# Kernel tuning notes

Measured on AMD Instinct MI355X. Metric: run time of the kernel, lower is better.

## Reference

```python
import jax, jax.numpy as jnp
import numpy as np

INPUT_SIZE = 4
HIDDEN_SIZE = 64
OUTPUT_SIZE = 40
BATCH = 4096
SEQ_LEN = 512


def setup_inputs() -> dict:
    key = jax.random.key(0)
    ks = jax.random.split(key, 7)
    s_ih = 1.0 / np.sqrt(HIDDEN_SIZE)
    x = jax.random.normal(ks[0], (BATCH, SEQ_LEN, INPUT_SIZE), dtype=jnp.float32)
    # PyTorch nn.RNN params, uniform(-1/sqrt(H), 1/sqrt(H))
    W_ih = jax.random.uniform(ks[1], (HIDDEN_SIZE, INPUT_SIZE), minval=-s_ih, maxval=s_ih, dtype=jnp.float32)
    W_hh = jax.random.uniform(ks[2], (HIDDEN_SIZE, HIDDEN_SIZE), minval=-s_ih, maxval=s_ih, dtype=jnp.float32)
    b_ih = jax.random.uniform(ks[3], (HIDDEN_SIZE,), minval=-s_ih, maxval=s_ih, dtype=jnp.float32)
    b_hh = jax.random.uniform(ks[4], (HIDDEN_SIZE,), minval=-s_ih, maxval=s_ih, dtype=jnp.float32)
    fc_W = jax.random.uniform(ks[5], (OUTPUT_SIZE, HIDDEN_SIZE), minval=-s_ih, maxval=s_ih, dtype=jnp.float32)
    fc_b = jax.random.uniform(ks[6], (OUTPUT_SIZE,), minval=-s_ih, maxval=s_ih, dtype=jnp.float32)
    return {"x": x, "W_ih": W_ih, "W_hh": W_hh, "b_ih": b_ih, "b_hh": b_hh, "fc_W": fc_W, "fc_b": fc_b}


def reference(x, W_ih, W_hh, b_ih, b_hh, fc_W, fc_b):
    B = x.shape[0]
    # Precompute input projections for all timesteps: [T, B, H]
    xp = jnp.einsum('bti,hi->tbh', x, W_ih) + (b_ih + b_hh)

    def step(h, xp_t):
        h = jnp.tanh(xp_t + h @ W_hh.T)
        return h, None

    h0 = jnp.zeros((B, HIDDEN_SIZE), dtype=x.dtype)
    h_last, _ = jax.lax.scan(step, h0, xp)
    # fc on last timestep hidden state
    return h_last @ fc_W.T + fc_b
```

## Files before the change

### kernel.cpp

```cpp
#include <hip/hip_runtime.h>
#include <math.h>

#define BATCH 4096
#define SEQ_T 512
#define ISZ   4
#define HID   64
#define OSZ   40
#define RPB   16

typedef __attribute__((ext_vector_type(8))) _Float16     half8;
typedef __attribute__((ext_vector_type(2))) _Float16     half2v;
typedef __attribute__((ext_vector_type(4))) float        float4v;
typedef __attribute__((ext_vector_type(2))) unsigned int uint2v;

static __device__ __forceinline__ half2v pk_f16(float a, float b) {
    return __builtin_bit_cast(half2v, __builtin_amdgcn_cvt_pkrtz(a, b));
}

static __device__ __forceinline__ float fast_tanh(float x) {
    float e = __builtin_amdgcn_exp2f(x * 2.885390081777927f);
    return fmaf(-2.0f, __builtin_amdgcn_rcpf(e + 1.0f), 1.0f);
}

#define LDS_BARRIER() asm volatile("s_waitcnt lgkmcnt(0)\n\ts_barrier" ::: "memory")

__global__ __launch_bounds__(256, 1)
void rnn_f16x2_kernel(const float* __restrict__ x,
                      const float* __restrict__ W_ih,
                      const float* __restrict__ W_hh,
                      const float* __restrict__ b_ih,
                      const float* __restrict__ b_hh,
                      const float* __restrict__ fc_W,
                      const float* __restrict__ fc_b,
                      float* __restrict__ out)
{
    __shared__ __attribute__((aligned(16))) _Float16 hterm[2][2][8][16][8];
    __shared__ __attribute__((aligned(16))) float hf[16][68];

    const int tid  = threadIdx.x;
    const int wv   = tid >> 6;
    const int lane = tid & 63;
    const int n    = lane & 15;
    const int q    = lane >> 4;
    const int blk0 = blockIdx.x * RPB;

    {
        unsigned int* p = (unsigned int*)hterm;
        #pragma unroll
        for (int i = tid; i < (int)(sizeof(hterm) / 4); i += 256) p[i] = 0u;
    }

    half8 A10, A11, A20, A21;
    {
        const float* wr = W_hh + (16 * wv + n) * HID;
        #pragma unroll
        for (int j = 0; j < 8; ++j) {
            float f0 = wr[     8 * q + j];
            float f1 = wr[32 + 8 * q + j];
            _Float16 h0 = (_Float16)f0; A10[j] = h0; A20[j] = (_Float16)(f0 - (float)h0);
            _Float16 h1 = (_Float16)f1; A11[j] = h1; A21[j] = (_Float16)(f1 - (float)h1);
        }
    }

    const int r0 = 16 * wv + 4 * q;
    float wih[4][4], bias[4];
    #pragma unroll
    for (int r = 0; r < 4; ++r) {
        bias[r] = b_ih[r0 + r] + b_hh[r0 + r];
        #pragma unroll
        for (int i = 0; i < ISZ; ++i) wih[r][i] = W_ih[(r0 + r) * ISZ + i];
    }

    const float* xrow = x + (size_t)(blk0 + n) * SEQ_T * ISZ;
    float4v xc  = *(const float4v*)(xrow);
    float4v xn1 = *(const float4v*)(xrow + ISZ);
    float4v xn2 = *(const float4v*)(xrow + 2 * ISZ);

    float p0 = bias[0], p1 = bias[1], p2 = bias[2], p3 = bias[3];
    #pragma unroll
    for (int i = 0; i < ISZ; ++i) {
        p0 = fmaf(xc[i], wih[0][i], p0);
        p1 = fmaf(xc[i], wih[1][i], p1);
        p2 = fmaf(xc[i], wih[2][i], p2);
        p3 = fmaf(xc[i], wih[3][i], p3);
    }

    const int gw = 2 * wv + (q >> 1);
    const int j0 = 4 * (q & 1);

    float hl0 = 0.f, hl1 = 0.f, hl2 = 0.f, hl3 = 0.f;

    __syncthreads();

#define MFMA16(A, B, C) __builtin_amdgcn_mfma_f32_16x16x32_f16((A), (B), (C), 0, 0, 0)
#define RNN_STEP(RB, WB, T)                                                    \
    {                                                                          \
        int tn = (T) + 3; if (tn > SEQ_T - 1) tn = SEQ_T - 1;                  \
        const float4v xf = *(const float4v*)(xrow + (size_t)tn * ISZ);         \
        half8 B10 = *(const half8*)&hterm[RB][0][    q][n][0];                 \
        half8 B11 = *(const half8*)&hterm[RB][0][4 + q][n][0];                 \
        half8 B20 = *(const half8*)&hterm[RB][1][    q][n][0];                 \
        half8 B21 = *(const half8*)&hterm[RB][1][4 + q][n][0];                 \
        float4v accA = {p0, p1, p2, p3};                                       \
        float4v accB = {0.f, 0.f, 0.f, 0.f};                                   \
        accA = MFMA16(A10, B10, accA);  accB = MFMA16(A11, B11, accB);         \
        accA = MFMA16(A10, B20, accA);  accB = MFMA16(A11, B21, accB);         \
        accA = MFMA16(A20, B10, accA);  accB = MFMA16(A21, B11, accB);         \
        hl0 = fast_tanh(accA[0] + accB[0]); hl1 = fast_tanh(accA[1] + accB[1]);\
        hl2 = fast_tanh(accA[2] + accB[2]); hl3 = fast_tanh(accA[3] + accB[3]);\
        half2v hi01 = pk_f16(hl0, hl1), hi23 = pk_f16(hl2, hl3);               \
        float s0 = hl0 - (float)hi01[0], s1 = hl1 - (float)hi01[1];            \
        float s2 = hl2 - (float)hi23[0], s3 = hl3 - (float)hi23[1];            \
        half2v lo01 = pk_f16(s0, s1), lo23 = pk_f16(s2, s3);                   \
        uint2v whi = { __builtin_bit_cast(unsigned int, hi01),                 \
                       __builtin_bit_cast(unsigned int, hi23) };               \
        uint2v wlo = { __builtin_bit_cast(unsigned int, lo01),                 \
                       __builtin_bit_cast(unsigned int, lo23) };               \
        *(uint2v*)&hterm[WB][0][gw][n][j0] = whi;                              \
        *(uint2v*)&hterm[WB][1][gw][n][j0] = wlo;                              \
        \
        p0 = bias[0]; p1 = bias[1]; p2 = bias[2]; p3 = bias[3];                \
        _Pragma("unroll")                                                      \
        for (int i = 0; i < ISZ; ++i) {                                        \
            p0 = fmaf(xn1[i], wih[0][i], p0);                                  \
            p1 = fmaf(xn1[i], wih[1][i], p1);                                  \
            p2 = fmaf(xn1[i], wih[2][i], p2);                                  \
            p3 = fmaf(xn1[i], wih[3][i], p3);                                  \
        }                                                                      \
        xn1 = xn2; xn2 = xf;                                                   \
        LDS_BARRIER();                                                         \
    }

    for (int t = 0; t < SEQ_T; t += 2) {
        RNN_STEP(0, 1, t)
        RNN_STEP(1, 0, t + 1)
    }
#undef RNN_STEP
#undef MFMA16

    {
        float4v hv = {hl0, hl1, hl2, hl3};
        *(float4v*)&hf[n][16 * wv + 4 * q] = hv;
    }
    __syncthreads();
    for (int it = tid; it < RPB * OSZ; it += 256) {
        const int b = it / OSZ;
        const int o = it - b * OSZ;
        const float* wo = fc_W + o * HID;
        float acc = fc_b[o];
        #pragma unroll
        for (int j = 0; j < HID; ++j)
            acc = fmaf(hf[b][j], wo[j], acc);
        out[(size_t)(blk0 + b) * OSZ + o] = acc;
    }
}

extern "C" void kernel_launch(void* const* d_in, const int* in_sizes, int n_in,
                              void* d_out, int out_size, void* d_ws, size_t ws_size,
                              hipStream_t stream) {
    const float* x    = (const float*)d_in[0];
    const float* W_ih = (const float*)d_in[1];
    const float* W_hh = (const float*)d_in[2];
    const float* b_ih = (const float*)d_in[3];
    const float* b_hh = (const float*)d_in[4];
    const float* fc_W = (const float*)d_in[5];
    const float* fc_b = (const float*)d_in[6];
    float* out = (float*)d_out;

    rnn_f16x2_kernel<<<BATCH / RPB, 256, 0, stream>>>(
        x, W_ih, W_hh, b_ih, b_hh, fc_W, fc_b, out);
}
```

Measured before the change: 231.3 us.

## Pack two independent batch chains per workgroup to interleave recurrence latency

Result: slower. 292.4 us (+26.4%).

```diff
diff --git a/kernel.cpp b/kernel.cpp
--- a/kernel.cpp
+++ b/kernel.cpp
@@ -7,6 +7,7 @@
 #define HID   64
 #define OSZ   40
 #define RPB   16
+#define NCH   2
 
 typedef __attribute__((ext_vector_type(8))) _Float16     half8;
 typedef __attribute__((ext_vector_type(2))) _Float16     half2v;
@@ -24,7 +25,7 @@
 
 #define LDS_BARRIER() asm volatile("s_waitcnt lgkmcnt(0)\n\ts_barrier" ::: "memory")
 
-__global__ __launch_bounds__(256, 1)
+__global__ __launch_bounds__(512, 1)
 void rnn_f16x2_kernel(const float* __restrict__ x,
                       const float* __restrict__ W_ih,
                       const float* __restrict__ W_hh,
@@ -34,20 +35,22 @@
                       const float* __restrict__ fc_b,
                       float* __restrict__ out)
 {
-    __shared__ __attribute__((aligned(16))) _Float16 hterm[2][2][8][16][8];
-    __shared__ __attribute__((aligned(16))) float hf[16][68];
+    __shared__ __attribute__((aligned(16))) _Float16 hterm[NCH][2][2][8][16][8];
+    __shared__ __attribute__((aligned(16))) float hf[NCH][16][68];
 
     const int tid  = threadIdx.x;
-    const int wv   = tid >> 6;
-    const int lane = tid & 63;
+    const int ch   = tid >> 8;
+    const int ctid = tid & 255;
+    const int wv   = ctid >> 6;
+    const int lane = ctid & 63;
     const int n    = lane & 15;
     const int q    = lane >> 4;
-    const int blk0 = blockIdx.x * RPB;
+    const int blk0 = blockIdx.x * (RPB * NCH) + ch * RPB;
 
     {
         unsigned int* p = (unsigned int*)hterm;
         #pragma unroll
-        for (int i = tid; i < (int)(sizeof(hterm) / 4); i += 256) p[i] = 0u;
+        for (int i = tid; i < (int)(sizeof(hterm) / 4); i += 512) p[i] = 0u;
     }
 
     half8 A10, A11, A20, A21;
@@ -97,10 +100,10 @@
     {                                                                          \
         int tn = (T) + 3; if (tn > SEQ_T - 1) tn = SEQ_T - 1;                  \
         const float4v xf = *(const float4v*)(xrow + (size_t)tn * ISZ);         \
-        half8 B10 = *(const half8*)&hterm[RB][0][    q][n][0];                 \
-        half8 B11 = *(const half8*)&hterm[RB][0][4 + q][n][0];                 \
-        half8 B20 = *(const half8*)&hterm[RB][1][    q][n][0];                 \
-        half8 B21 = *(const half8*)&hterm[RB][1][4 + q][n][0];                 \
+        half8 B10 = *(const half8*)&hterm[ch][RB][0][    q][n][0];             \
+        half8 B11 = *(const half8*)&hterm[ch][RB][0][4 + q][n][0];             \
+        half8 B20 = *(const half8*)&hterm[ch][RB][1][    q][n][0];             \
+        half8 B21 = *(const half8*)&hterm[ch][RB][1][4 + q][n][0];             \
         float4v accA = {p0, p1, p2, p3};                                       \
         float4v accB = {0.f, 0.f, 0.f, 0.f};                                   \
         accA = MFMA16(A10, B10, accA);  accB = MFMA16(A11, B11, accB);         \
@@ -116,8 +119,8 @@
                        __builtin_bit_cast(unsigned int, hi23) };               \
         uint2v wlo = { __builtin_bit_cast(unsigned int, lo01),                 \
                        __builtin_bit_cast(unsigned int, lo23) };               \
-        *(uint2v*)&hterm[WB][0][gw][n][j0] = whi;                              \
-        *(uint2v*)&hterm[WB][1][gw][n][j0] = wlo;                              \
+        *(uint2v*)&hterm[ch][WB][0][gw][n][j0] = whi;                          \
+        *(uint2v*)&hterm[ch][WB][1][gw][n][j0] = wlo;                          \
         \
         p0 = bias[0]; p1 = bias[1]; p2 = bias[2]; p3 = bias[3];                \
         _Pragma("unroll")                                                      \
@@ -140,17 +143,17 @@
 
     {
         float4v hv = {hl0, hl1, hl2, hl3};
-        *(float4v*)&hf[n][16 * wv + 4 * q] = hv;
+        *(float4v*)&hf[ch][n][16 * wv + 4 * q] = hv;
     }
     __syncthreads();
-    for (int it = tid; it < RPB * OSZ; it += 256) {
+    for (int it = ctid; it < RPB * OSZ; it += 256) {
         const int b = it / OSZ;
         const int o = it - b * OSZ;
         const float* wo = fc_W + o * HID;
         float acc = fc_b[o];
         #pragma unroll
         for (int j = 0; j < HID; ++j)
-            acc = fmaf(hf[b][j], wo[j], acc);
+            acc = fmaf(hf[ch][b][j], wo[j], acc);
         out[(size_t)(blk0 + b) * OSZ + o] = acc;
     }
 }
@@ -167,6 +170,6 @@
     const float* fc_b = (const float*)d_in[6];
     float* out = (float*)d_out;
 
-    rnn_f16x2_kernel<<<BATCH / RPB, 256, 0, stream>>>(
+    rnn_f16x2_kernel<<<BATCH / (RPB * NCH), 512, 0, stream>>>(
         x, W_ih, W_hh, b_ih, b_hh, fc_W, fc_b, out);
 }
```
